# Kernel optimization log

Hardware: AMD Instinct MI355X
Metric: run time of the kernel (lower is better)

Reference implementation:

```python
import jax, jax.numpy as jnp
import numpy as np

N = 20000      # nodes
E = 320000     # edges (before self-loops)
F_IN = 50      # PPI num_features
C1 = 256       # per-head channels, conv1/conv2
H1 = 4         # heads, conv1/conv2
C3 = 121       # PPI num_classes, conv3 per-head channels
H3 = 6         # heads, conv3 (concat=False -> mean)


def gat_conv(x, src, dst, W, a_src, a_dst, b, heads, ch, concat, n):
    """PyG-style GATConv with self-loops already included in (src, dst).
    Messages flow src -> dst; softmax is over incoming edges of each dst node."""
    h = (x @ W).reshape(n, heads, ch)                      # [N, H, C]
    es = jnp.sum(h * a_src, axis=-1)                       # [N, H]
    ed = jnp.sum(h * a_dst, axis=-1)                       # [N, H]
    e = jax.nn.leaky_relu(es[src] + ed[dst], 0.2)          # [E', H]
    m = jax.ops.segment_max(e, dst, num_segments=n)        # stable softmax per dst
    e = jnp.exp(e - m[dst])
    denom = jax.ops.segment_sum(e, dst, num_segments=n)
    alpha = e / jnp.maximum(denom[dst], 1e-16)             # [E', H]
    out = jax.ops.segment_sum(alpha[:, :, None] * h[src], dst, num_segments=n)  # [N, H, C]
    out = out.reshape(n, heads * ch) if concat else out.mean(axis=1)
    return out + b


def setup_inputs() -> dict:
    key = jax.random.key(0)
    ks = jax.random.split(key, 16)

    def p(k, shape, fan_in):
        return (jax.random.normal(k, shape, jnp.float32) / np.float32(np.sqrt(fan_in)))

    x = jax.random.normal(ks[0], (N, F_IN), jnp.float32)
    edge_index = jax.random.randint(ks[1], (2, E), 0, N, dtype=jnp.int64)
    D1 = H1 * C1  # 1024
    return dict(
        x=x, edge_index=edge_index,
        W1=p(ks[2], (F_IN, D1), F_IN), a1s=p(ks[3], (H1, C1), C1), a1d=p(ks[4], (H1, C1), C1), b1=jnp.zeros((D1,), jnp.float32),
        Wl1=p(ks[5], (F_IN, D1), F_IN), bl1=jnp.zeros((D1,), jnp.float32),
        W2=p(ks[6], (D1, D1), D1), a2s=p(ks[7], (H1, C1), C1), a2d=p(ks[8], (H1, C1), C1), b2=jnp.zeros((D1,), jnp.float32),
        Wl2=p(ks[9], (D1, D1), D1), bl2=jnp.zeros((D1,), jnp.float32),
        W3=p(ks[10], (D1, H3 * C3), D1), a3s=p(ks[11], (H3, C3), C3), a3d=p(ks[12], (H3, C3), C3), b3=jnp.zeros((C3,), jnp.float32),
        Wl3=p(ks[13], (D1, C3), D1), bl3=jnp.zeros((C3,), jnp.float32),
    )


def reference(x, edge_index, W1, a1s, a1d, b1, Wl1, bl1, W2, a2s, a2d, b2, Wl2, bl2, W3, a3s, a3d, b3, Wl3, bl3):
    n = x.shape[0]
    loop = jnp.arange(n, dtype=edge_index.dtype)           # PyG GATConv adds self-loops
    src = jnp.concatenate([edge_index[0], loop])
    dst = jnp.concatenate([edge_index[1], loop])
    x1 = jax.nn.elu(gat_conv(x, src, dst, W1, a1s, a1d, b1, H1, C1, True, n) + x @ Wl1 + bl1)
    x2 = jax.nn.elu(gat_conv(x1, src, dst, W2, a2s, a2d, b2, H1, C1, True, n) + x1 @ Wl2 + bl2)
    out = gat_conv(x2, src, dst, W3, a3s, a3d, b3, H3, C3, False, n) + x2 @ Wl3 + bl3
    return out
```

## Files before the change

kernel.cpp:

```cpp
#include <hip/hip_runtime.h>
#include <hip/hip_bf16.h>
#include <math.h>

typedef __bf16 bf16;
typedef __attribute__((ext_vector_type(4))) __bf16 bf16x4;
typedef __attribute__((ext_vector_type(8))) __bf16 bf16x8;
typedef __attribute__((ext_vector_type(4))) float f32x4;

#define N_NODES 20000
#define N_EDGES 320000
#define E2 (N_EDGES + N_NODES)
#define F_IN 50
#define D1 1024
#define NP12 2048
#define NP3 896
#define SG 2048
#define KA 320

#define PO_A1S 0
#define PO_A1D 1024
#define PO_B1  2048
#define PO_BL1 3072
#define PO_A2S 4096
#define PO_A2D 5120
#define PO_B2  6144
#define PO_BL2 7168
#define PO_A3S 8192
#define PO_A3D 8918
#define PO_B3  9644
#define PO_BL3 9765
#define PO_END 9886

__device__ __forceinline__ int clampi(int v, int lo, int hi)
{
    return v < lo ? lo : (v > hi ? hi : v);
}

__device__ __forceinline__ float loadf(const void* p, long idx, int isb)
{
    return isb ? (float)((const bf16*)p)[idx] : ((const float*)p)[idx];
}

__device__ __forceinline__ int loadei(const int* ei, long idx, int i64)
{
    return i64 ? ei[2 * idx] : ei[idx];
}

__global__ void k_detect(const int* __restrict__ ei,
                         const unsigned short* __restrict__ xw,
                         int* __restrict__ flags)
{
    if (blockIdx.x != 0 || threadIdx.x != 0) return;
    int allz = 1;
    for (int i = 0; i < 128; ++i)
        if (ei[2 * i + 1] != 0) { allz = 0; break; }
    int inr = 0;
    for (int i = 0; i < 128; ++i) {
        int e = (xw[2 * i] >> 7) & 0xFF;
        if (e >= 100 && e <= 140) inr++;
    }
    flags[0] = allz;
    flags[1] = (inr >= 64) ? 1 : 0;
}

template <bool BACT>
__global__ __launch_bounds__(256) void k_gemm(const bf16* __restrict__ A,
                                              const bf16* __restrict__ Bt,
                                              bf16* __restrict__ C,
                                              int M, int K, int lda, int ldb, int ldc,
                                              int mtiles, int ntiles,
                                              const bf16* __restrict__ bias)
{
    __shared__ bf16 As[128 * 64];
    __shared__ bf16 Bs[128 * 64];

    int id = blockIdx.x;
    int gfull = mtiles >> 3;
    int base  = gfull * 8 * ntiles;
    int x, y;
    if (id < base) {
        int gsz = 8 * ntiles;
        int g = id / gsz;
        int r = id - g * gsz;
        x = g * 8 + (r & 7);
        y = r >> 3;
    } else {
        int rem = mtiles - (gfull << 3);
        int r = id - base;
        x = (gfull << 3) + r % rem;
        y = r / rem;
    }
    const int m0 = x * 128;
    const int n0 = y * 128;

    const int tid  = threadIdx.x;
    const int wave = tid >> 6;
    const int lane = tid & 63;
    const int wm   = (wave >> 1) * 64;
    const int wn   = (wave & 1) * 64;
    const int frow  = lane & 15;

    const int srow = wave * 32 + (lane >> 3);
    const int scol = (((lane & 7) ^ (lane >> 3)) * 8);

    f32x4 acc[4][4];
#pragma unroll
    for (int i = 0; i < 4; ++i)
#pragma unroll
        for (int j = 0; j < 4; ++j)
#pragma unroll
            for (int r = 0; r < 4; ++r) acc[i][j][r] = 0.f;

    for (int k0 = 0; k0 < K; k0 += 64) {
#pragma unroll
        for (int i = 0; i < 4; ++i) {
            int ra = srow + i * 8;
            int ga = m0 + ra; if (ga > M - 1) ga = M - 1;
            __builtin_amdgcn_global_load_lds(
                (const __attribute__((address_space(1))) void*)(A + (size_t)ga * lda + k0 + scol),
                (__attribute__((address_space(3))) void*)(As + wave * 2048 + i * 512),
                16, 0, 0);
            int gb = n0 + ra;
            __builtin_amdgcn_global_load_lds(
                (const __attribute__((address_space(1))) void*)(Bt + (size_t)gb * ldb + k0 + scol),
                (__attribute__((address_space(3))) void*)(Bs + wave * 2048 + i * 512),
                16, 0, 0);
        }
        __syncthreads();
#pragma unroll
        for (int kk = 0; kk < 2; ++kk) {
            const int coff = (((kk * 4 + (lane >> 4)) ^ (frow & 7)) << 3);
            bf16x8 af[4], bfr[4];
#pragma unroll
            for (int i = 0; i < 4; ++i) {
                af[i]  = *(const bf16x8*)(As + (wm + i * 16 + frow) * 64 + coff);
                bfr[i] = *(const bf16x8*)(Bs + (wn + i * 16 + frow) * 64 + coff);
            }
#pragma unroll
            for (int i = 0; i < 4; ++i)
#pragma unroll
                for (int j = 0; j < 4; ++j)
                    acc[i][j] = __builtin_amdgcn_mfma_f32_16x16x32_bf16(af[i], bfr[j], acc[i][j], 0, 0, 0);
        }
        __syncthreads();
    }

#pragma unroll
    for (int i = 0; i < 4; ++i) {
#pragma unroll
        for (int j = 0; j < 4; ++j) {
            int rbase = m0 + wm + i * 16 + (lane >> 4) * 4;
            int col   = n0 + wn + j * 16 + frow;
            if constexpr (BACT) {
                float bv = (float)bias[col];
#pragma unroll
                for (int r = 0; r < 4; ++r) {
                    int row = rbase + r;
                    if (row < M) {
                        float v = acc[i][j][r] + bv;
                        v = (v > 0.f) ? v : (expf(v) - 1.f);
                        C[(size_t)row * ldc + col] = (bf16)v;
                    }
                }
            } else {
#pragma unroll
                for (int r = 0; r < 4; ++r) {
                    int row = rbase + r;
                    if (row < M) C[(size_t)row * ldc + col] = (bf16)acc[i][j][r];
                }
            }
        }
    }
}

__global__ void k_padx(const void* __restrict__ x, bf16* __restrict__ A2,
                       const int* __restrict__ flags)
{
    int idx = blockIdx.x * 256 + threadIdx.x;
    if (idx >= N_NODES * 64) return;
    int isb = flags[1];
    int n = idx >> 6, k = idx & 63;
    A2[(size_t)n * KA + 256 + k] = (k < F_IN) ? (bf16)loadf(x, (long)n * F_IN + k, isb)
                                              : (bf16)0.f;
}

__global__ __launch_bounds__(256) void k_veca(const void* __restrict__ W1,
                                              const void* __restrict__ a1s,
                                              const void* __restrict__ a1d,
                                              const void* __restrict__ b1,
                                              const void* __restrict__ bl1,
                                              float* __restrict__ ws, float* __restrict__ wd,
                                              bf16* __restrict__ bsum,
                                              const int* __restrict__ flags)
{
    const int isb = flags[1];
    const int k = blockIdx.x;
    const int h = threadIdx.x >> 6;
    const int c0 = threadIdx.x & 63;
    float s = 0.f, d = 0.f;
    if (k < F_IN) {
        for (int c = c0; c < 256; c += 64) {
            float wv = loadf(W1, (long)k * D1 + h * 256 + c, isb);
            s += wv * loadf(a1s, h * 256 + c, isb);
            d += wv * loadf(a1d, h * 256 + c, isb);
        }
    }
#pragma unroll
    for (int off = 32; off; off >>= 1) {
        s += __shfl_xor(s, off);
        d += __shfl_xor(d, off);
    }
    if (c0 == 0) { ws[k * 4 + h] = s; wd[k * 4 + h] = d; }
    if (k < 4) {
        int j = k * 256 + threadIdx.x;
        bsum[j] = (bf16)(loadf(b1, j, isb) + loadf(bl1, j, isb));
    }
}

__global__ void k_wfuse1(const void* __restrict__ W1, const void* __restrict__ Wl1,
                         bf16* __restrict__ Bt, const int* __restrict__ flags)
{
    int idx = blockIdx.x * 256 + threadIdx.x;
    if (idx >= D1 * KA) return;
    int isb = flags[1];
    int j = idx / KA;
    int kp = idx - j * KA;
    float v = 0.f;
    if (kp < 256) {
        int hp = kp >> 6, k = kp & 63;
        if ((j >> 8) == hp && k < F_IN) v = loadf(W1, (long)k * D1 + j, isb);
    } else {
        int k = kp - 256;
        if (k < F_IN) v = loadf(Wl1, (long)k * D1 + j, isb);
    }
    Bt[idx] = (bf16)v;
}

__global__ __launch_bounds__(256) void k_wcatT(const void* __restrict__ Wa,
                                               const void* __restrict__ Wb,
                                               bf16* __restrict__ Bt,
                                               int split, int da, int db,
                                               const int* __restrict__ flags)
{
    __shared__ bf16 T[64][65];
    const int isb = flags[1];
    const int k0 = blockIdx.x * 64;
    const int n0 = blockIdx.y * 64;
    const int r = threadIdx.x >> 6;
    const int c = threadIdx.x & 63;
    const int n = n0 + c;
#pragma unroll
    for (int kk = 0; kk < 16; ++kk) {
        int k = k0 + r + kk * 4;
        float v = 0.f;
        if (n < split)           v = loadf(Wa, (long)k * da + n, isb);
        else if (n < split + db) v = loadf(Wb, (long)k * db + (n - split), isb);
        T[r + kk * 4][c] = (bf16)v;
    }
    __syncthreads();
#pragma unroll
    for (int kk = 0; kk < 16; ++kk) {
        int nn = r + kk * 4;
        Bt[(size_t)(n0 + nn) * 1024 + k0 + c] = T[c][nn];
    }
}

struct P12 { const void* s[12]; };

__global__ void k_params(P12 ps, bf16* __restrict__ pool, const int* __restrict__ flags)
{
    const int off[13] = {PO_A1S, PO_A1D, PO_B1, PO_BL1, PO_A2S, PO_A2D, PO_B2,
                         PO_BL2, PO_A3S, PO_A3D, PO_B3, PO_BL3, PO_END};
    int idx = blockIdx.x * 256 + threadIdx.x;
    if (idx >= PO_END) return;
    int isb = flags[1];
    int seg = 0;
    while (idx >= off[seg + 1]) seg++;
    pool[idx] = (bf16)loadf(ps.s[seg], idx - off[seg], isb);
}

__global__ void k_count(const int* __restrict__ ei, int* __restrict__ cnt,
                        const int* __restrict__ flags)
{
    int e = blockIdx.x * 256 + threadIdx.x;
    if (e >= E2) return;
    int i64 = flags[0];
    int d = (e < N_EDGES) ? loadei(ei, (long)N_EDGES + e, i64) : (e - N_EDGES);
    d = clampi(d, 0, N_NODES - 1);
    atomicAdd(&cnt[d], 1);
}

__global__ __launch_bounds__(256) void k_scan(const int* __restrict__ cnt, int* __restrict__ rp)
{
    __shared__ int ssum[256];
    int tid = threadIdx.x;
    const int chunk = (N_NODES + 255) / 256;
    int lo = tid * chunk;
    int hi = lo + chunk; if (hi > N_NODES) hi = N_NODES;
    int s = 0;
    for (int i = lo; i < hi; ++i) s += cnt[i];
    ssum[tid] = s;
    __syncthreads();
    if (tid == 0) {
        int run = 0;
        for (int i = 0; i < 256; ++i) { int t = ssum[i]; ssum[i] = run; run += t; }
        rp[N_NODES] = run;
    }
    __syncthreads();
    int run = ssum[tid];
    for (int i = lo; i < hi; ++i) { rp[i] = run; run += cnt[i]; }
}

__global__ void k_copy(const int* __restrict__ rp, int* __restrict__ cur)
{
    int i = blockIdx.x * 256 + threadIdx.x;
    if (i < N_NODES) cur[i] = rp[i];
}

__global__ void k_fill(const int* __restrict__ ei, int* __restrict__ cur,
                       int* __restrict__ ss, const int* __restrict__ flags)
{
    int e = blockIdx.x * 256 + threadIdx.x;
    if (e >= E2) return;
    int i64 = flags[0];
    int s, d;
    if (e < N_EDGES) {
        s = loadei(ei, e, i64);
        d = loadei(ei, (long)N_EDGES + e, i64);
    } else {
        s = e - N_EDGES; d = s;
    }
    s = clampi(s, 0, N_NODES - 1);
    d = clampi(d, 0, N_NODES - 1);
    int pos = atomicAdd(&cur[d], 1);
    if (pos >= 0 && pos < E2) ss[pos] = s;
}

__global__ __launch_bounds__(256) void k_logits1(const bf16* __restrict__ A2,
                                                 const float* __restrict__ ws,
                                                 const float* __restrict__ wd,
                                                 float* __restrict__ es, float* __restrict__ ed)
{
    const int wave = threadIdx.x >> 6;
    const int lane = threadIdx.x & 63;
    const int n = blockIdx.x * 4 + wave;
    if (n >= N_NODES) return;
    float xv = (float)A2[(size_t)n * KA + 256 + lane];
    f32x4 wsv = *(const f32x4*)(ws + lane * 4);
    f32x4 wdv = *(const f32x4*)(wd + lane * 4);
    float s[4], d[4];
#pragma unroll
    for (int h = 0; h < 4; ++h) { s[h] = xv * wsv[h]; d[h] = xv * wdv[h]; }
#pragma unroll
    for (int off = 32; off; off >>= 1)
#pragma unroll
        for (int h = 0; h < 4; ++h) {
            s[h] += __shfl_xor(s[h], off);
            d[h] += __shfl_xor(d[h], off);
        }
    if (lane == 0) {
#pragma unroll
        for (int h = 0; h < 4; ++h) { es[n * 4 + h] = s[h]; ed[n * 4 + h] = d[h]; }
    }
}

__global__ __launch_bounds__(256) void k_aggx(bf16* __restrict__ A2,
                                              const float* __restrict__ es,
                                              const float* __restrict__ ed,
                                              const int* __restrict__ rp,
                                              const int* __restrict__ ss)
{
    __shared__ float smx[4], sinv[4], sed[4];
    __shared__ float sal[64 * 4];
    __shared__ int   ssrc[64];

    const int n   = blockIdx.x;
    const int tid = threadIdx.x;
    int r0 = clampi(rp[n], 0, E2);
    int r1 = clampi(rp[n + 1], r0, E2);
    const int deg = r1 - r0;

    const int sw = tid >> 5, ln = tid & 31;
    if (sw < 4) {
        int h = sw;
        float edn = ed[n * 4 + h];
        float mx = -1e30f;
        for (int e = ln; e < deg; e += 32) {
            int s = clampi(ss[r0 + e], 0, N_NODES - 1);
            float w = es[s * 4 + h] + edn;
            w = (w > 0.f) ? w : 0.2f * w;
            mx = fmaxf(mx, w);
        }
#pragma unroll
        for (int off = 16; off; off >>= 1) mx = fmaxf(mx, __shfl_xor(mx, off, 32));
        float sm = 0.f;
        for (int e = ln; e < deg; e += 32) {
            int s = clampi(ss[r0 + e], 0, N_NODES - 1);
            float w = es[s * 4 + h] + edn;
            w = (w > 0.f) ? w : 0.2f * w;
            sm += expf(w - mx);
        }
#pragma unroll
        for (int off = 16; off; off >>= 1) sm += __shfl_xor(sm, off, 32);
        if (ln == 0) { smx[h] = mx; sinv[h] = 1.f / fmaxf(sm, 1e-16f); sed[h] = edn; }
    }
    __syncthreads();

    const int k  = tid & 63;
    const int hh = tid >> 6;
    float acc = 0.f;

    for (int e0 = 0; e0 < deg; e0 += 64) {
        int ce = min(64, deg - e0);
        __syncthreads();
        if (tid < ce * 4) {
            int e = tid >> 2, h = tid & 3;
            int s = clampi(ss[r0 + e0 + e], 0, N_NODES - 1);
            float w = es[s * 4 + h] + sed[h];
            w = (w > 0.f) ? w : 0.2f * w;
            sal[e * 4 + h] = expf(w - smx[h]) * sinv[h];
            if (h == 0) ssrc[e] = s;
        }
        __syncthreads();
        for (int e = 0; e < ce; ++e) {
            int s = ssrc[e];
            float xv = (float)A2[(size_t)s * KA + 256 + k];
            acc += sal[e * 4 + hh] * xv;
        }
    }
    A2[(size_t)n * KA + hh * 64 + k] = (bf16)acc;
}

template <int H, int C>
__global__ __launch_bounds__(256) void k_logits(const bf16* __restrict__ G,
                                                const bf16* __restrict__ as_,
                                                const bf16* __restrict__ ad_,
                                                float* __restrict__ es, float* __restrict__ ed)
{
    const int wave = threadIdx.x >> 6;
    const int lane = threadIdx.x & 63;
    const int n = blockIdx.x * 4 + wave;
    if (n >= N_NODES) return;

#pragma unroll
    for (int h = 0; h < H; ++h) {
        float s = 0.f, d = 0.f;
        if constexpr (C == 256) {
            bf16x4 g  = *(const bf16x4*)(G + (size_t)n * SG + h * 256 + lane * 4);
            bf16x4 av = *(const bf16x4*)(as_ + h * 256 + lane * 4);
            bf16x4 dv = *(const bf16x4*)(ad_ + h * 256 + lane * 4);
#pragma unroll
            for (int j = 0; j < 4; ++j) {
                float gv = (float)g[j];
                s += gv * (float)av[j];
                d += gv * (float)dv[j];
            }
        } else {
            for (int c = lane; c < C; c += 64) {
                float hv = (float)G[(size_t)n * SG + h * C + c];
                s += hv * (float)as_[h * C + c];
                d += hv * (float)ad_[h * C + c];
            }
        }
#pragma unroll
        for (int off = 32; off; off >>= 1) {
            s += __shfl_xor(s, off);
            d += __shfl_xor(d, off);
        }
        if (lane == 0) { es[n * H + h] = s; ed[n * H + h] = d; }
    }
}

template <int H, int C, bool MEAN, bool ELU, bool EXTOUT>
__global__ __launch_bounds__(256) void k_agg(const bf16* __restrict__ G,
                                             const bf16* __restrict__ S,
                                             const float* __restrict__ es,
                                             const float* __restrict__ ed,
                                             const int* __restrict__ rp,
                                             const int* __restrict__ ss,
                                             const bf16* __restrict__ bgat,
                                             const bf16* __restrict__ bskip,
                                             void* __restrict__ out, int sout,
                                             const int* __restrict__ flags)
{
    constexpr int D  = H * C;
    constexpr int NV = (D + 3) / 4;
    constexpr int CH = 256;
    __shared__ float smx[H], sinv[H], sed[H];
    __shared__ float sal[CH * H];
    __shared__ int   ssrc[CH];

    const int n   = blockIdx.x;
    const int tid = threadIdx.x;
    int r0 = clampi(rp[n], 0, E2);
    int r1 = clampi(rp[n + 1], r0, E2);
    const int deg = r1 - r0;

    const int sw = tid >> 5, ln = tid & 31;
    for (int h = sw; h < H; h += 8) {
        float edn = ed[n * H + h];
        float mx = -1e30f;
        for (int e = ln; e < deg; e += 32) {
            int s = clampi(ss[r0 + e], 0, N_NODES - 1);
            float w = es[s * H + h] + edn;
            w = (w > 0.f) ? w : 0.2f * w;
            mx = fmaxf(mx, w);
        }
#pragma unroll
        for (int off = 16; off; off >>= 1) mx = fmaxf(mx, __shfl_xor(mx, off, 32));
        float sm = 0.f;
        for (int e = ln; e < deg; e += 32) {
            int s = clampi(ss[r0 + e], 0, N_NODES - 1);
            float w = es[s * H + h] + edn;
            w = (w > 0.f) ? w : 0.2f * w;
            sm += expf(w - mx);
        }
#pragma unroll
        for (int off = 16; off; off >>= 1) sm += __shfl_xor(sm, off, 32);
        if (ln == 0) { smx[h] = mx; sinv[h] = 1.f / fmaxf(sm, 1e-16f); sed[h] = edn; }
    }
    __syncthreads();

    const int c0 = tid * 4;
    const int hA = (c0 < D) ? (c0 / C) : 0;
    const int hB = (c0 + 3 < D) ? ((c0 + 3) / C) : hA;
    int hj1 = ((c0 + 1 < D) ? ((c0 + 1) / C) : hA) == hA;
    int hj2 = ((c0 + 2 < D) ? ((c0 + 2) / C) : hA) == hA;
    const bool active = (tid < NV);

    float acc[4] = {0.f, 0.f, 0.f, 0.f};

    for (int e0 = 0; e0 < deg; e0 += CH) {
        int ce = min(CH, deg - e0);
        __syncthreads();
        for (int t = tid; t < ce * H; t += 256) {
            int e = t / H, h = t - e * H;
            int s = clampi(ss[r0 + e0 + e], 0, N_NODES - 1);
            float w = es[s * H + h] + sed[h];
            w = (w > 0.f) ? w : 0.2f * w;
            sal[e * H + h] = expf(w - smx[h]) * sinv[h];
            if (h == 0) ssrc[e] = s;
        }
        __syncthreads();
        if (active) {
            for (int eb = 0; eb < ce; eb += 4) {
                int idx[4]; float zm[4];
#pragma unroll
                for (int p = 0; p < 4; ++p) {
                    int e = eb + p;
                    idx[p] = (e < ce) ? e : eb;
                    zm[p]  = (e < ce) ? 1.f : 0.f;
                }
                int sg[4];
#pragma unroll
                for (int p = 0; p < 4; ++p) sg[p] = ssrc[idx[p]];
                bf16x4 g[4];
#pragma unroll
                for (int p = 0; p < 4; ++p)
                    g[p] = *(const bf16x4*)(G + (size_t)sg[p] * SG + c0);
                if constexpr (C % 4 == 0) {
                    float a[4];
#pragma unroll
                    for (int p = 0; p < 4; ++p) a[p] = sal[idx[p] * H + hA] * zm[p];
#pragma unroll
                    for (int p = 0; p < 4; ++p)
#pragma unroll
                        for (int j = 0; j < 4; ++j)
                            acc[j] += a[p] * (float)g[p][j];
                } else {
                    float aL[4], aH[4];
#pragma unroll
                    for (int p = 0; p < 4; ++p) {
                        aL[p] = sal[idx[p] * H + hA] * zm[p];
                        aH[p] = sal[idx[p] * H + hB] * zm[p];
                    }
#pragma unroll
                    for (int p = 0; p < 4; ++p) {
                        acc[0] += aL[p] * (float)g[p][0];
                        acc[1] += (hj1 ? aL[p] : aH[p]) * (float)g[p][1];
                        acc[2] += (hj2 ? aL[p] : aH[p]) * (float)g[p][2];
                        acc[3] += aH[p] * (float)g[p][3];
                    }
                }
            }
        }
    }

    const int outbf = EXTOUT ? flags[1] : 1;

    if constexpr (!MEAN) {
        if (active) {
            bf16x4 bg = *(const bf16x4*)(bgat + c0);
            bf16x4 sk = *(const bf16x4*)(S + (size_t)n * SG + c0);
            bf16x4 bs = *(const bf16x4*)(bskip + c0);
            bf16x4 ov;
#pragma unroll
            for (int j = 0; j < 4; ++j) {
                float v = acc[j] + (float)bg[j] + (float)sk[j] + (float)bs[j];
                if (ELU) v = (v > 0.f) ? v : (expf(v) - 1.f);
                ov[j] = (bf16)v;
            }
            *(bf16x4*)((bf16*)out + (size_t)n * sout + c0) = ov;
        }
    } else {
        __shared__ float sagg[D];
        if (active) {
#pragma unroll
            for (int j = 0; j < 4; ++j) {
                int c = c0 + j;
                if (c < D) sagg[c] = acc[j];
            }
        }
        __syncthreads();
        for (int c = tid; c < C; c += 256) {
            float v = 0.f;
#pragma unroll
            for (int h = 0; h < H; ++h) v += sagg[h * C + c];
            v *= (1.f / H);
            v += (float)bgat[c] + (float)S[(size_t)n * SG + c] + (float)bskip[c];
            if (outbf) ((bf16*)out)[(size_t)n * sout + c] = (bf16)v;
            else       ((float*)out)[(size_t)n * sout + c] = v;
        }
    }
}

extern "C" void kernel_launch(void* const* d_in, const int* in_sizes, int n_in,
                              void* d_out, int out_size, void* d_ws, size_t ws_size,
                              hipStream_t stream)
{
    const void* x   = d_in[0];
    const int*  ei  = (const int*)d_in[1];
    const void* W1  = d_in[2];
    const void* Wl1 = d_in[6];
    const void* W2  = d_in[8];
    const void* Wl2 = d_in[12];
    const void* W3  = d_in[14];
    const void* Wl3 = d_in[18];

    P12 ps;
    ps.s[0] = d_in[3];  ps.s[1] = d_in[4];  ps.s[2] = d_in[5];  ps.s[3] = d_in[7];
    ps.s[4] = d_in[9];  ps.s[5] = d_in[10]; ps.s[6] = d_in[11]; ps.s[7] = d_in[13];
    ps.s[8] = d_in[15]; ps.s[9] = d_in[16]; ps.s[10] = d_in[17]; ps.s[11] = d_in[19];

    char* w = (char*)d_ws;
    auto alloc = [&](size_t bytes) {
        char* p = w;
        w += (bytes + 255) & ~(size_t)255;
        return p;
    };
    int*   flags = (int*)alloc(64);
    int*   cnt   = (int*)alloc((size_t)N_NODES * 4);
    int*   rp    = (int*)alloc((size_t)(N_NODES + 1) * 4);
    int*   cur   = (int*)alloc((size_t)N_NODES * 4);
    int*   ss    = (int*)alloc((size_t)E2 * 4);
    float* es    = (float*)alloc((size_t)N_NODES * 6 * 4);
    float* ed    = (float*)alloc((size_t)N_NODES * 6 * 4);
    bf16*  pool  = (bf16*)alloc((size_t)PO_END * 2);
    float* ws1   = (float*)alloc((size_t)64 * 4 * 4);
    float* wd1   = (float*)alloc((size_t)64 * 4 * 4);
    bf16*  bsum  = (bf16*)alloc((size_t)D1 * 2);
    bf16*  Bt    = (bf16*)alloc((size_t)NP12 * 1024 * 2);
    bf16*  X     = (bf16*)alloc((size_t)N_NODES * D1 * 2);
    bf16*  WS    = (bf16*)alloc((size_t)N_NODES * SG * 2);
    bf16*  A2    = WS;

    k_detect<<<1, 64, 0, stream>>>(ei, (const unsigned short*)x, flags);

    hipMemsetAsync(cnt, 0, N_NODES * 4, stream);
    k_count<<<(E2 + 255) / 256, 256, 0, stream>>>(ei, cnt, flags);
    k_scan<<<1, 256, 0, stream>>>(cnt, rp);
    k_copy<<<(N_NODES + 255) / 256, 256, 0, stream>>>(rp, cur);
    k_fill<<<(E2 + 255) / 256, 256, 0, stream>>>(ei, cur, ss, flags);

    k_params<<<(PO_END + 255) / 256, 256, 0, stream>>>(ps, pool, flags);

    const dim3 blk(256);
    const int MT = (N_NODES + 127) / 128;

    k_veca<<<64, 256, 0, stream>>>(W1, ps.s[0], ps.s[1], ps.s[2], ps.s[3],
                                   ws1, wd1, bsum, flags);
    k_padx<<<(N_NODES * 64 + 255) / 256, 256, 0, stream>>>(x, A2, flags);
    k_wfuse1<<<(D1 * KA + 255) / 256, 256, 0, stream>>>(W1, Wl1, Bt, flags);
    k_logits1<<<N_NODES / 4, 256, 0, stream>>>(A2, ws1, wd1, es, ed);
    k_aggx<<<N_NODES, 256, 0, stream>>>(A2, es, ed, rp, ss);
    k_gemm<true><<<MT * (D1 / 128), blk, 0, stream>>>(A2, Bt, X, N_NODES, KA, KA, KA, D1,
                                                      MT, D1 / 128, bsum);

    k_wcatT<<<dim3(16, NP12 / 64), blk, 0, stream>>>(W2, Wl2, Bt, 1024, 1024, 1024, flags);
    k_gemm<false><<<MT * (NP12 / 128), blk, 0, stream>>>(X, Bt, WS, N_NODES, 1024, 1024, 1024, SG,
                                                         MT, NP12 / 128, nullptr);
    k_logits<4, 256><<<N_NODES / 4, 256, 0, stream>>>(WS, pool + PO_A2S, pool + PO_A2D, es, ed);
    k_agg<4, 256, false, true, false><<<N_NODES, 256, 0, stream>>>(
        WS, WS + D1, es, ed, rp, ss, pool + PO_B2, pool + PO_BL2, X, D1, flags);

    k_wcatT<<<dim3(16, NP3 / 64), blk, 0, stream>>>(W3, Wl3, Bt, 726, 726, 121, flags);
    k_gemm<false><<<MT * (NP3 / 128), blk, 0, stream>>>(X, Bt, WS, N_NODES, 1024, 1024, 1024, SG,
                                                        MT, NP3 / 128, nullptr);
    k_logits<6, 121><<<N_NODES / 4, 256, 0, stream>>>(WS, pool + PO_A3S, pool + PO_A3D, es, ed);
    k_agg<6, 121, true, false, true><<<N_NODES, 256, 0, stream>>>(
        WS, WS + 726, es, ed, rp, ss, pool + PO_B3, pool + PO_BL3, d_out, 121, flags);
}
```

Before: 654.0 us.

## Use online softmax and split edges across two thread groups in GAT aggregation

Replaces the two-pass softmax statistics (max pass and sum pass over all incoming edges) with an online softmax that rescales running accumulators per 256-edge chunk, so each edge's logit is computed once. The feature loop now uses 8-wide bf16 loads with two 128-thread groups processing alternating edge quads, and their partials are reduced through shared memory before normalization. This removes the redundant passes over es gathers and the serial per-head warp loop, at the cost of extra syncs, a shared reduction buffer, and rescaling work.

```diff
diff --git a/kernel.cpp b/kernel.cpp
--- a/kernel.cpp
+++ b/kernel.cpp
@@ -483,12 +483,17 @@
                                              void* __restrict__ out, int sout,
                                              const int* __restrict__ flags)
 {
-    constexpr int D  = H * C;
-    constexpr int NV = (D + 3) / 4;
-    constexpr int CH = 256;
-    __shared__ float smx[H], sinv[H], sed[H];
-    __shared__ float sal[CH * H];
+    constexpr int  D     = H * C;
+    constexpr int  NT8   = (D + 7) / 8;
+    constexpr int  CH    = 256;
+    constexpr bool CDIV8 = (C % 8 == 0);
+    static_assert(NT8 <= 128, "row must fit one 128-thread group");
+
+    __shared__ float s_f[H];
+    __shared__ float s_inv[H];
+    __shared__ float sal[H * CH];
     __shared__ int   ssrc[CH];
+    __shared__ float sred[D];
 
     const int n   = blockIdx.x;
     const int tid = threadIdx.x;
@@ -497,125 +502,143 @@
     const int deg = r1 - r0;
 
     const int sw = tid >> 5, ln = tid & 31;
-    for (int h = sw; h < H; h += 8) {
-        float edn = ed[n * H + h];
-        float mx = -1e30f;
-        for (int e = ln; e < deg; e += 32) {
-            int s = clampi(ss[r0 + e], 0, N_NODES - 1);
-            float w = es[s * H + h] + edn;
-            w = (w > 0.f) ? w : 0.2f * w;
-            mx = fmaxf(mx, w);
-        }
-#pragma unroll
-        for (int off = 16; off; off >>= 1) mx = fmaxf(mx, __shfl_xor(mx, off, 32));
-        float sm = 0.f;
-        for (int e = ln; e < deg; e += 32) {
-            int s = clampi(ss[r0 + e], 0, N_NODES - 1);
-            float w = es[s * H + h] + edn;
-            w = (w > 0.f) ? w : 0.2f * w;
-            sm += expf(w - mx);
-        }
-#pragma unroll
-        for (int off = 16; off; off >>= 1) sm += __shfl_xor(sm, off, 32);
-        if (ln == 0) { smx[h] = mx; sinv[h] = 1.f / fmaxf(sm, 1e-16f); sed[h] = edn; }
-    }
-    __syncthreads();
-
-    const int c0 = tid * 4;
-    const int hA = (c0 < D) ? (c0 / C) : 0;
-    const int hB = (c0 + 3 < D) ? ((c0 + 3) / C) : hA;
-    int hj1 = ((c0 + 1 < D) ? ((c0 + 1) / C) : hA) == hA;
-    int hj2 = ((c0 + 2 < D) ? ((c0 + 2) / C) : hA) == hA;
-    const bool active = (tid < NV);
-
-    float acc[4] = {0.f, 0.f, 0.f, 0.f};
+    const float edn = (sw < H) ? ed[n * H + sw] : 0.f;
+    float m_run = -1e30f, d_run = 0.f;
+
+    const int  grp = tid >> 7;
+    const int  tg  = tid & 127;
+    const bool act = (tg < NT8);
+    const int  c0  = tg * 8;
+    int hA = c0 / C;        if (hA > H - 1) hA = H - 1;
+    int hB = (c0 + 7) / C;  if (hB > H - 1) hB = H - 1;
+    bool jA[8];
+#pragma unroll
+    for (int j = 0; j < 8; ++j)
+        jA[j] = CDIV8 ? true : (((c0 + j) / C) == hA);
+
+    float acc[8] = {0.f, 0.f, 0.f, 0.f, 0.f, 0.f, 0.f, 0.f};
 
     for (int e0 = 0; e0 < deg; e0 += CH) {
-        int ce = min(CH, deg - e0);
+        const int ce = min(CH, deg - e0);
         __syncthreads();
-        for (int t = tid; t < ce * H; t += 256) {
-            int e = t / H, h = t - e * H;
-            int s = clampi(ss[r0 + e0 + e], 0, N_NODES - 1);
-            float w = es[s * H + h] + sed[h];
-            w = (w > 0.f) ? w : 0.2f * w;
-            sal[e * H + h] = expf(w - smx[h]) * sinv[h];
-            if (h == 0) ssrc[e] = s;
+        if (sw < H) {
+            float w[8]; int sv[8];
+            float mc = -1e30f;
+#pragma unroll
+            for (int i = 0; i < 8; ++i) {
+                const int e = ln + (i << 5);
+                w[i] = -1e30f; sv[i] = 0;
+                if (e < ce) {
+                    const int s = clampi(ss[r0 + e0 + e], 0, N_NODES - 1);
+                    sv[i] = s;
+                    float v = es[s * H + sw] + edn;
+                    v = (v > 0.f) ? v : 0.2f * v;
+                    w[i] = v;
+                    mc = fmaxf(mc, v);
+                }
+            }
+#pragma unroll
+            for (int off = 16; off; off >>= 1) mc = fmaxf(mc, __shfl_xor(mc, off, 32));
+            const float mn = fmaxf(m_run, mc);
+            const float f  = expf(m_run - mn);
+            float dsum = 0.f;
+#pragma unroll
+            for (int i = 0; i < 8; ++i) {
+                const int e = ln + (i << 5);
+                if (e < ce) {
+                    const float p = expf(w[i] - mn);
+                    sal[sw * CH + e] = p;
+                    dsum += p;
+                    if (sw == 0) ssrc[e] = sv[i];
+                }
+            }
+#pragma unroll
+            for (int off = 16; off; off >>= 1) dsum += __shfl_xor(dsum, off, 32);
+            d_run = d_run * f + dsum;
+            m_run = mn;
+            if (ln == 0) s_f[sw] = f;
         }
         __syncthreads();
-        if (active) {
-            for (int eb = 0; eb < ce; eb += 4) {
+        if (act) {
+            if (e0 > 0) {
+                const float fA = s_f[hA], fB = s_f[hB];
+#pragma unroll
+                for (int j = 0; j < 8; ++j) acc[j] *= (CDIV8 || jA[j]) ? fA : fB;
+            }
+            for (int eb = grp * 4; eb < ce; eb += 8) {
                 int idx[4]; float zm[4];
 #pragma unroll
                 for (int p = 0; p < 4; ++p) {
-                    int e = eb + p;
-                    idx[p] = (e < ce) ? e : eb;
+                    const int e = eb + p;
+                    idx[p] = (e < ce) ? e : 0;
                     zm[p]  = (e < ce) ? 1.f : 0.f;
                 }
                 int sg[4];
 #pragma unroll
                 for (int p = 0; p < 4; ++p) sg[p] = ssrc[idx[p]];
-                bf16x4 g[4];
+                bf16x8 g[4];
 #pragma unroll
                 for (int p = 0; p < 4; ++p)
-                    g[p] = *(const bf16x4*)(G + (size_t)sg[p] * SG + c0);
-                if constexpr (C % 4 == 0) {
+                    g[p] = *(const bf16x8*)(G + (size_t)sg[p] * SG + c0);
+                if constexpr (CDIV8) {
                     float a[4];
 #pragma unroll
-                    for (int p = 0; p < 4; ++p) a[p] = sal[idx[p] * H + hA] * zm[p];
+                    for (int p = 0; p < 4; ++p) a[p] = sal[hA * CH + idx[p]] * zm[p];
 #pragma unroll
                     for (int p = 0; p < 4; ++p)
 #pragma unroll
-                        for (int j = 0; j < 4; ++j)
-                            acc[j] += a[p] * (float)g[p][j];
+                        for (int j = 0; j < 8; ++j) acc[j] += a[p] * (float)g[p][j];
                 } else {
-                    float aL[4], aH[4];
 #pragma unroll
                     for (int p = 0; p < 4; ++p) {
-                        aL[p] = sal[idx[p] * H + hA] * zm[p];
-                        aH[p] = sal[idx[p] * H + hB] * zm[p];
-                    }
-#pragma unroll
-                    for (int p = 0; p < 4; ++p) {
-                        acc[0] += aL[p] * (float)g[p][0];
-                        acc[1] += (hj1 ? aL[p] : aH[p]) * (float)g[p][1];
-                        acc[2] += (hj2 ? aL[p] : aH[p]) * (float)g[p][2];
-                        acc[3] += aH[p] * (float)g[p][3];
+                        const float aL = sal[hA * CH + idx[p]] * zm[p];
+                        const float aH_ = sal[hB * CH + idx[p]] * zm[p];
+#pragma unroll
+                        for (int j = 0; j < 8; ++j)
+                            acc[j] += (jA[j] ? aL : aH_) * (float)g[p][j];
                     }
                 }
             }
         }
     }
 
+    if (sw < H && ln == 0) s_inv[sw] = 1.f / fmaxf(d_run, 1e-16f);
+
+    __syncthreads();
+    if (grp == 0 && act) {
+#pragma unroll
+        for (int j = 0; j < 8; ++j) if (c0 + j < D) sred[c0 + j] = acc[j];
+    }
+    __syncthreads();
+    if (grp == 1 && act) {
+#pragma unroll
+        for (int j = 0; j < 8; ++j) if (c0 + j < D) sred[c0 + j] += acc[j];
+    }
+    __syncthreads();
+
     const int outbf = EXTOUT ? flags[1] : 1;
 
     if constexpr (!MEAN) {
-        if (active) {
-            bf16x4 bg = *(const bf16x4*)(bgat + c0);
-            bf16x4 sk = *(const bf16x4*)(S + (size_t)n * SG + c0);
-            bf16x4 bs = *(const bf16x4*)(bskip + c0);
-            bf16x4 ov;
-#pragma unroll
-            for (int j = 0; j < 4; ++j) {
-                float v = acc[j] + (float)bg[j] + (float)sk[j] + (float)bs[j];
+        if (grp == 0 && act) {
+            const float iA = s_inv[hA], iB = s_inv[hB];
+            bf16x8 bg = *(const bf16x8*)(bgat + c0);
+            bf16x8 sk = *(const bf16x8*)(S + (size_t)n * SG + c0);
+            bf16x8 bs = *(const bf16x8*)(bskip + c0);
+            bf16x8 ov;
+#pragma unroll
+            for (int j = 0; j < 8; ++j) {
+                float v = sred[c0 + j] * ((CDIV8 || jA[j]) ? iA : iB)
+                        + (float)bg[j] + (float)sk[j] + (float)bs[j];
                 if (ELU) v = (v > 0.f) ? v : (expf(v) - 1.f);
                 ov[j] = (bf16)v;
             }
-            *(bf16x4*)((bf16*)out + (size_t)n * sout + c0) = ov;
+            *(bf16x8*)((bf16*)out + (size_t)n * sout + c0) = ov;
         }
     } else {
-        __shared__ float sagg[D];
-        if (active) {
-#pragma unroll
-            for (int j = 0; j < 4; ++j) {
-                int c = c0 + j;
-                if (c < D) sagg[c] = acc[j];
-            }
-        }
-        __syncthreads();
         for (int c = tid; c < C; c += 256) {
             float v = 0.f;
 #pragma unroll
-            for (int h = 0; h < H; ++h) v += sagg[h * C + c];
+            for (int h = 0; h < H; ++h) v += sred[h * C + c] * s_inv[h];
             v *= (1.f / H);
             v += (float)bgat[c] + (float)S[(size_t)n * SG + c] + (float)bskip[c];
             if (outbf) ((bf16*)out)[(size_t)n * sout + c] = (bf16)v;
```

Result: no change. 666.9 us (+2.0%).
